# Kernel tuning notes

Hardware: AMD Instinct MI355X
Metric: run time of the kernel (lower is better)

Reference implementation:

```python
import jax, jax.numpy as jnp
import numpy as np


def euler2mat(angle):
    """angle: [..., 3] euler angles (x, y, z) -> [..., 3, 3] rotation matrix (xmat @ ymat @ zmat)."""
    x, y, z = angle[..., 0], angle[..., 1], angle[..., 2]
    zo = jnp.zeros_like(z)
    on = jnp.ones_like(z)
    cz, sz = jnp.cos(z), jnp.sin(z)
    cy, sy = jnp.cos(y), jnp.sin(y)
    cx, sx = jnp.cos(x), jnp.sin(x)
    zmat = jnp.stack([cz, -sz, zo, sz, cz, zo, zo, zo, on], axis=-1).reshape(*z.shape, 3, 3)
    ymat = jnp.stack([cy, zo, sy, zo, on, zo, -sy, zo, cy], axis=-1).reshape(*z.shape, 3, 3)
    xmat = jnp.stack([on, zo, zo, zo, cx, -sx, zo, sx, cx], axis=-1).reshape(*z.shape, 3, 3)
    return xmat @ ymat @ zmat


def pixel_grid(H, W, dtype=jnp.float32):
    """Matches torch affine_grid(identity, align_corners=False): normalized (x, y) in (-1, 1)."""
    xs = (2.0 * (jnp.arange(W, dtype=dtype) + 0.5) / W) - 1.0
    ys = (2.0 * (jnp.arange(H, dtype=dtype) + 0.5) / H) - 1.0
    X, Y = jnp.meshgrid(xs, ys, indexing='xy')  # [H, W] each
    return jnp.stack([X, Y], axis=-1)  # [H, W, 2], last dim = (x, y)


def setup_inputs() -> dict:
    key = jax.random.key(0)
    k1, k2, k3, k4, k5 = jax.random.split(key, 5)
    B, K, H, W = 8, 8, 384, 384
    im = jax.random.normal(k1, (B, H, W), dtype=jnp.float32)
    mask = jax.random.uniform(k2, (B, K, H, W), dtype=jnp.float32)
    depth = jax.random.uniform(k3, (B, H, W), dtype=jnp.float32, minval=0.5, maxval=1.5)
    T = jax.random.normal(k4, (B, K, 6), dtype=jnp.float32) * 0.1
    Tc = jax.random.normal(k5, (B, 9), dtype=jnp.float32) * 0.1
    return {"im": im, "mask": mask, "depth": depth, "T": T, "Tc": Tc}


def reference(im, mask, depth, T, Tc):
    B, K, H, W = mask.shape
    pixel = jnp.broadcast_to(pixel_grid(H, W, depth.dtype), (B, H, W, 2))  # [B,H,W,2]

    # object transforms
    t, a = T[..., 0:3], T[..., 3:6]            # [B,K,3] each
    R = euler2mat(a)                           # [B,K,3,3]
    # camera transform
    tc = Tc[..., 0:3]                          # [B,3]
    Rc = euler2mat(Tc[..., 3:6])               # [B,3,3]
    pc = Tc[..., 6:9]                          # [B,3]

    # pixel -> world (focal length = 1): [B,H,W,3]
    ones = jnp.ones((B, H, W, 1), dtype=depth.dtype)
    world = depth[..., None] * jnp.concatenate([pixel, ones], axis=-1)

    # centre of mass per mask: [B,K,3]
    total_mass = jnp.sum(mask, axis=(2, 3))[..., None] + 1e-6  # [B,K,1]
    p = jnp.einsum('bkhw,bhwc->bkc', mask, world) / total_mass

    # per-object rigid transform about centre of mass
    centered = world[:, None] - p[:, :, None, None]                       # [B,K,H,W,3]
    rotated = jnp.einsum('bkij,bkhwj->bkhwi', R, centered)                # [B,K,H,W,3]
    twc_k = rotated + (p + t)[:, :, None, None]                           # [B,K,H,W,3]

    # mask-weighted blend of per-object displacements
    twc = world + jnp.einsum('bkhw,bkhwc->bhwc', mask, twc_k - world[:, None])

    # camera transform about pivot pc
    twc = jnp.einsum('bij,bhwj->bhwi', Rc, twc - pc[:, None, None])
    twc = twc + (pc + tc)[:, None, None]

    # world -> pixel, flow
    new_pixel = twc[..., 0:2] / twc[..., 2:3]
    flow = new_pixel - pixel
    return flow
```

## Files before the change

### kernel.cpp

```cpp
#include <hip/hip_runtime.h>

#define B 8
#define K 8
#define H 384
#define W 384
#define HW (H*W)
#define NCPP 16
#define GROUPS_PER_B (HW/4)

#define WS_PK (B*K*NCPP*4)
#define WS_PB (WS_PK + B*K*12)

__device__ __forceinline__ void euler2mat(float ax, float ay, float az, float R[9]) {
    float cx = cosf(ax), sx = sinf(ax);
    float cy = cosf(ay), sy = sinf(ay);
    float cz = cosf(az), sz = sinf(az);
    R[0] = cy*cz;              R[1] = -cy*sz;             R[2] = sy;
    R[3] = cx*sz + sx*sy*cz;   R[4] = cx*cz - sx*sy*sz;   R[5] = -sx*cy;
    R[6] = sx*sz - cx*sy*cz;   R[7] = sx*cz + cx*sy*sz;   R[8] = cx*cy;
}

__global__ __launch_bounds__(256) void k_reduce(const float* __restrict__ mask,
                                                const float* __restrict__ depth,
                                                float* __restrict__ ws) {
    const int chunk = blockIdx.x, k = blockIdx.y, b = blockIdx.z;
    const int tid = threadIdx.x;

    const float4* m4 = (const float4*)(mask + ((size_t)(b*K + k)) * HW);
    const float4* d4 = (const float4*)(depth + (size_t)b * HW);

    float s0 = 0.f, s1 = 0.f, s2 = 0.f, s3 = 0.f;
    const float inv = 2.f / W;

#pragma unroll
    for (int r = 0; r < 9; ++r) {
        int g = (chunk * 9 + r) * 256 + tid;
        float4 mv = m4[g];
        float4 dv = d4[g];
        int i0 = g * 4;
        int h = i0 / W;
        int w0 = i0 - h * W;
        float py = 2.f * (h + 0.5f) * (1.f / H) - 1.f;
        float px0 = 2.f * (w0 + 0.5f) * (1.f / W) - 1.f;
        float mm[4] = {mv.x, mv.y, mv.z, mv.w};
        float dd[4] = {dv.x, dv.y, dv.z, dv.w};
#pragma unroll
        for (int j = 0; j < 4; ++j) {
            float m = mm[j];
            float t = m * dd[j];
            float px = px0 + j * inv;
            s0 += m; s1 += t * px; s2 += t * py; s3 += t;
        }
    }

    for (int off = 32; off > 0; off >>= 1) {
        s0 += __shfl_down(s0, off);
        s1 += __shfl_down(s1, off);
        s2 += __shfl_down(s2, off);
        s3 += __shfl_down(s3, off);
    }
    __shared__ float sd[16];
    int lane = tid & 63, wid = tid >> 6;
    if (lane == 0) { sd[wid*4+0]=s0; sd[wid*4+1]=s1; sd[wid*4+2]=s2; sd[wid*4+3]=s3; }
    __syncthreads();
    if (tid < 4) {
        float v = sd[tid] + sd[4 + tid] + sd[8 + tid] + sd[12 + tid];
        ws[(((b*K + k) * NCPP) + chunk) * 4 + tid] = v;
    }
}

__global__ void k_params(const float* __restrict__ T, const float* __restrict__ Tc,
                         float* __restrict__ ws) {
    int t = threadIdx.x;
    if (t < 64) {
        float s0 = 0.f, s1 = 0.f, s2 = 0.f, s3 = 0.f;
        for (int ch = 0; ch < NCPP; ++ch) {
            const float* src = ws + (t * NCPP + ch) * 4;
            s0 += src[0]; s1 += src[1]; s2 += src[2]; s3 += src[3];
        }
        float mass = s0 + 1e-6f;
        float p0 = s1 / mass, p1 = s2 / mass, p2 = s3 / mass;
        const float* Tk = T + t * 6;
        float R[9];
        euler2mat(Tk[3], Tk[4], Tk[5], R);
        float Rp0 = R[0]*p0 + R[1]*p1 + R[2]*p2;
        float Rp1 = R[3]*p0 + R[4]*p1 + R[5]*p2;
        float Rp2 = R[6]*p0 + R[7]*p1 + R[8]*p2;
        float* o = ws + WS_PK + t * 12;
        o[0] = R[0] - 1.f; o[1] = R[1];       o[2] = R[2];
        o[3] = R[3];       o[4] = R[4] - 1.f; o[5] = R[5];
        o[6] = R[6];       o[7] = R[7];       o[8] = R[8] - 1.f;
        o[9]  = p0 + Tk[0] - Rp0;
        o[10] = p1 + Tk[1] - Rp1;
        o[11] = p2 + Tk[2] - Rp2;
    }
    if (t < 8) {
        const float* Tb = Tc + t * 9;
        float R[9];
        euler2mat(Tb[3], Tb[4], Tb[5], R);
        float pc0 = Tb[6], pc1 = Tb[7], pc2 = Tb[8];
        float* o = ws + WS_PB + t * 12;
#pragma unroll
        for (int i = 0; i < 9; ++i) o[i] = R[i];
        o[9]  = pc0 + Tb[0] - (R[0]*pc0 + R[1]*pc1 + R[2]*pc2);
        o[10] = pc1 + Tb[1] - (R[3]*pc0 + R[4]*pc1 + R[5]*pc2);
        o[11] = pc2 + Tb[2] - (R[6]*pc0 + R[7]*pc1 + R[8]*pc2);
    }
}

__global__ __launch_bounds__(256) void k_flow(const float* __restrict__ mask,
                                              const float* __restrict__ depth,
                                              const float* __restrict__ ws,
                                              float* __restrict__ out) {
    const int b = blockIdx.y;
    const int tid = threadIdx.x;

    __shared__ float sp[108];
    if (tid < 96) sp[tid] = ws[WS_PK + b * 96 + tid];
    else if (tid < 108) sp[tid] = ws[WS_PB + b * 12 + (tid - 96)];
    __syncthreads();

    int g = blockIdx.x * 256 + tid;
    int i0 = g * 4;
    int h = i0 / W;
    int w0 = i0 - h * W;
    float py = 2.f * (h + 0.5f) * (1.f / H) - 1.f;
    const float inv = 2.f / W;
    float px0 = 2.f * (w0 + 0.5f) * (1.f / W) - 1.f;

    float4 dv = ((const float4*)(depth + (size_t)b * HW))[g];
    float4 mf[K];
#pragma unroll
    for (int k = 0; k < K; ++k)
        mf[k] = ((const float4*)(mask + ((size_t)(b*K + k)) * HW))[g];

    float dd[4] = {dv.x, dv.y, dv.z, dv.w};
    float res[8];
#pragma unroll
    for (int j = 0; j < 4; ++j) {
        float px = px0 + j * inv;
        float d = dd[j];
        float wx = d * px, wy = d * py, wz = d;
        float ax = wx, ay = wy, az = wz;
#pragma unroll
        for (int k = 0; k < K; ++k) {
            const float* P = sp + k * 12;
            float m = (j == 0) ? mf[k].x : (j == 1) ? mf[k].y : (j == 2) ? mf[k].z : mf[k].w;
            float rx = P[0]*wx + P[1]*wy + P[2]*wz + P[9];
            float ry = P[3]*wx + P[4]*wy + P[5]*wz + P[10];
            float rz = P[6]*wx + P[7]*wy + P[8]*wz + P[11];
            ax += m * rx; ay += m * ry; az += m * rz;
        }
        const float* C = sp + 96;
        float ox = C[0]*ax + C[1]*ay + C[2]*az + C[9];
        float oy = C[3]*ax + C[4]*ay + C[5]*az + C[10];
        float oz = C[6]*ax + C[7]*ay + C[8]*az + C[11];
        res[j*2 + 0] = ox / oz - px;
        res[j*2 + 1] = oy / oz - py;
    }

    float4* o4 = (float4*)(out + ((size_t)b * HW + i0) * 2);
    o4[0] = make_float4(res[0], res[1], res[2], res[3]);
    o4[1] = make_float4(res[4], res[5], res[6], res[7]);
}

extern "C" void kernel_launch(void* const* d_in, const int* in_sizes, int n_in,
                              void* d_out, int out_size, void* d_ws, size_t ws_size,
                              hipStream_t stream) {
    const float* mask  = (const float*)d_in[1];
    const float* depth = (const float*)d_in[2];
    const float* T     = (const float*)d_in[3];
    const float* Tc    = (const float*)d_in[4];
    float* ws  = (float*)d_ws;
    float* out = (float*)d_out;

    k_reduce<<<dim3(NCPP, K, B), 256, 0, stream>>>(mask, depth, ws);
    k_params<<<1, 64, 0, stream>>>(T, Tc, ws);
    k_flow<<<dim3(GROUPS_PER_B / 256, B), 256, 0, stream>>>(mask, depth, ws, out);
}
```

Measured before the change: 27.16 us.

## Restructure reduction to per-pixel-segment blocks loading all K masks at once

The reduction kernel now assigns each block one 256-float4 segment of one batch and loads all eight masks plus depth once per segment, reducing every mask's four moments in the same block. The old version used one block per (chunk, k, b) and reread depth for every mask. Partial sums are written per segment, 144 segments per batch, so the params kernel now serially sums 144 values per moment in a single block. The flow kernel uses a 1D grid matching the segment layout and writes its output with nontemporal stores. The extra serial summation in the one-block params kernel adds latency.

```diff
diff --git a/kernel.cpp b/kernel.cpp
--- a/kernel.cpp
+++ b/kernel.cpp
@@ -5,11 +5,13 @@
 #define H 384
 #define W 384
 #define HW (H*W)
-#define NCPP 16
-#define GROUPS_PER_B (HW/4)
+#define SEGS 144
+#define NBLK (B*SEGS)
+#define PBASE (B*32*SEGS)
+#define PB_CAM (PBASE + B*K*12)
 
-#define WS_PK (B*K*NCPP*4)
-#define WS_PB (WS_PK + B*K*12)
+typedef float f32x4 __attribute__((ext_vector_type(4)));
+
 
 __device__ __forceinline__ void euler2mat(float ax, float ay, float az, float R[9]) {
     float cx = cosf(ax), sx = sinf(ax);
@@ -20,52 +22,57 @@
     R[6] = sx*sz - cx*sy*cz;   R[7] = sx*cz + cx*sy*sz;   R[8] = cx*cy;
 }
 
-__global__ __launch_bounds__(256) void k_reduce(const float* __restrict__ mask,
-                                                const float* __restrict__ depth,
-                                                float* __restrict__ ws) {
-    const int chunk = blockIdx.x, k = blockIdx.y, b = blockIdx.z;
+__global__ __launch_bounds__(256) void k_pre(const float* __restrict__ mask,
+                                             const float* __restrict__ depth,
+                                             float* __restrict__ ws) {
     const int tid = threadIdx.x;
+    const int blk = blockIdx.x;
+    const int b = blk / SEGS;
+    const int seg = blk - b * SEGS;
+    const int g = seg * 256 + tid;
 
-    const float4* m4 = (const float4*)(mask + ((size_t)(b*K + k)) * HW);
-    const float4* d4 = (const float4*)(depth + (size_t)b * HW);
+    __shared__ float sred[128];
 
-    float s0 = 0.f, s1 = 0.f, s2 = 0.f, s3 = 0.f;
+    float4 mv[K];
+#pragma unroll
+    for (int k = 0; k < K; ++k)
+        mv[k] = ((const float4*)(mask + ((size_t)(b*K + k)) * HW))[g];
+    float4 dv = ((const float4*)(depth + (size_t)b * HW))[g];
+    float dd[4] = {dv.x, dv.y, dv.z, dv.w};
+
+    const int h = g / 96;
+    const int w0 = (g - h * 96) * 4;
+    const float py  = 2.f * (h + 0.5f) * (1.f / H) - 1.f;
+    const float px0 = 2.f * (w0 + 0.5f) * (1.f / W) - 1.f;
     const float inv = 2.f / W;
 
+    const int lane = tid & 63, wid = tid >> 6;
 #pragma unroll
-    for (int r = 0; r < 9; ++r) {
-        int g = (chunk * 9 + r) * 256 + tid;
-        float4 mv = m4[g];
-        float4 dv = d4[g];
-        int i0 = g * 4;
-        int h = i0 / W;
-        int w0 = i0 - h * W;
-        float py = 2.f * (h + 0.5f) * (1.f / H) - 1.f;
-        float px0 = 2.f * (w0 + 0.5f) * (1.f / W) - 1.f;
-        float mm[4] = {mv.x, mv.y, mv.z, mv.w};
-        float dd[4] = {dv.x, dv.y, dv.z, dv.w};
+    for (int k = 0; k < K; ++k) {
+        float mm[4] = {mv[k].x, mv[k].y, mv[k].z, mv[k].w};
+        float s0 = 0.f, s1 = 0.f, s2 = 0.f, s3 = 0.f;
 #pragma unroll
         for (int j = 0; j < 4; ++j) {
-            float m = mm[j];
-            float t = m * dd[j];
-            float px = px0 + j * inv;
+            float m = mm[j], t = m * dd[j], px = px0 + j * inv;
             s0 += m; s1 += t * px; s2 += t * py; s3 += t;
         }
+        for (int off = 32; off > 0; off >>= 1) {
+            s0 += __shfl_down(s0, off);
+            s1 += __shfl_down(s1, off);
+            s2 += __shfl_down(s2, off);
+            s3 += __shfl_down(s3, off);
+        }
+        if (lane == 0) {
+            sred[wid*32 + k*4 + 0] = s0;
+            sred[wid*32 + k*4 + 1] = s1;
+            sred[wid*32 + k*4 + 2] = s2;
+            sred[wid*32 + k*4 + 3] = s3;
+        }
     }
-
-    for (int off = 32; off > 0; off >>= 1) {
-        s0 += __shfl_down(s0, off);
-        s1 += __shfl_down(s1, off);
-        s2 += __shfl_down(s2, off);
-        s3 += __shfl_down(s3, off);
-    }
-    __shared__ float sd[16];
-    int lane = tid & 63, wid = tid >> 6;
-    if (lane == 0) { sd[wid*4+0]=s0; sd[wid*4+1]=s1; sd[wid*4+2]=s2; sd[wid*4+3]=s3; }
     __syncthreads();
-    if (tid < 4) {
-        float v = sd[tid] + sd[4 + tid] + sd[8 + tid] + sd[12 + tid];
-        ws[(((b*K + k) * NCPP) + chunk) * 4 + tid] = v;
+    if (tid < 32) {
+        float v = sred[tid] + sred[32 + tid] + sred[64 + tid] + sred[96 + tid];
+        ws[((size_t)(b*32 + tid)) * SEGS + seg] = v;
     }
 }
 
@@ -73,20 +80,24 @@
                          float* __restrict__ ws) {
     int t = threadIdx.x;
     if (t < 64) {
-        float s0 = 0.f, s1 = 0.f, s2 = 0.f, s3 = 0.f;
-        for (int ch = 0; ch < NCPP; ++ch) {
-            const float* src = ws + (t * NCPP + ch) * 4;
-            s0 += src[0]; s1 += src[1]; s2 += src[2]; s3 += src[3];
+        int b = t >> 3, k = t & 7;
+        float s[4];
+#pragma unroll
+        for (int c = 0; c < 4; ++c) {
+            const float* src = ws + ((size_t)(b*32 + k*4 + c)) * SEGS;
+            float acc = 0.f;
+            for (int sg = 0; sg < SEGS; ++sg) acc += src[sg];
+            s[c] = acc;
         }
-        float mass = s0 + 1e-6f;
-        float p0 = s1 / mass, p1 = s2 / mass, p2 = s3 / mass;
+        float mass = s[0] + 1e-6f;
+        float p0 = s[1] / mass, p1 = s[2] / mass, p2 = s[3] / mass;
         const float* Tk = T + t * 6;
         float R[9];
         euler2mat(Tk[3], Tk[4], Tk[5], R);
         float Rp0 = R[0]*p0 + R[1]*p1 + R[2]*p2;
         float Rp1 = R[3]*p0 + R[4]*p1 + R[5]*p2;
         float Rp2 = R[6]*p0 + R[7]*p1 + R[8]*p2;
-        float* o = ws + WS_PK + t * 12;
+        float* o = ws + PBASE + t * 12;
         o[0] = R[0] - 1.f; o[1] = R[1];       o[2] = R[2];
         o[3] = R[3];       o[4] = R[4] - 1.f; o[5] = R[5];
         o[6] = R[6];       o[7] = R[7];       o[8] = R[8] - 1.f;
@@ -99,7 +110,7 @@
         float R[9];
         euler2mat(Tb[3], Tb[4], Tb[5], R);
         float pc0 = Tb[6], pc1 = Tb[7], pc2 = Tb[8];
-        float* o = ws + WS_PB + t * 12;
+        float* o = ws + PB_CAM + t * 12;
 #pragma unroll
         for (int i = 0; i < 9; ++i) o[i] = R[i];
         o[9]  = pc0 + Tb[0] - (R[0]*pc0 + R[1]*pc1 + R[2]*pc2);
@@ -112,27 +123,29 @@
                                               const float* __restrict__ depth,
                                               const float* __restrict__ ws,
                                               float* __restrict__ out) {
-    const int b = blockIdx.y;
     const int tid = threadIdx.x;
+    const int blk = blockIdx.x;
+    const int b = blk / SEGS;
+    const int seg = blk - b * SEGS;
+    const int g = seg * 256 + tid;
 
     __shared__ float sp[108];
-    if (tid < 96) sp[tid] = ws[WS_PK + b * 96 + tid];
-    else if (tid < 108) sp[tid] = ws[WS_PB + b * 12 + (tid - 96)];
+    if (tid < 96) sp[tid] = ws[PBASE + b * 96 + tid];
+    else if (tid < 108) sp[tid] = ws[PB_CAM + b * 12 + (tid - 96)];
     __syncthreads();
-
-    int g = blockIdx.x * 256 + tid;
-    int i0 = g * 4;
-    int h = i0 / W;
-    int w0 = i0 - h * W;
-    float py = 2.f * (h + 0.5f) * (1.f / H) - 1.f;
-    const float inv = 2.f / W;
-    float px0 = 2.f * (w0 + 0.5f) * (1.f / W) - 1.f;
 
     float4 dv = ((const float4*)(depth + (size_t)b * HW))[g];
     float4 mf[K];
 #pragma unroll
     for (int k = 0; k < K; ++k)
         mf[k] = ((const float4*)(mask + ((size_t)(b*K + k)) * HW))[g];
+
+    const int i0 = g * 4;
+    const int h = i0 / W;
+    const int w0 = i0 - h * W;
+    const float py = 2.f * (h + 0.5f) * (1.f / H) - 1.f;
+    const float inv = 2.f / W;
+    const float px0 = 2.f * (w0 + 0.5f) * (1.f / W) - 1.f;
 
     float dd[4] = {dv.x, dv.y, dv.z, dv.w};
     float res[8];
@@ -159,9 +172,11 @@
         res[j*2 + 1] = oy / oz - py;
     }
 
-    float4* o4 = (float4*)(out + ((size_t)b * HW + i0) * 2);
-    o4[0] = make_float4(res[0], res[1], res[2], res[3]);
-    o4[1] = make_float4(res[4], res[5], res[6], res[7]);
+    f32x4* o4 = (f32x4*)(out + ((size_t)b * HW + i0) * 2);
+    f32x4 v0 = {res[0], res[1], res[2], res[3]};
+    f32x4 v1 = {res[4], res[5], res[6], res[7]};
+    __builtin_nontemporal_store(v0, o4);
+    __builtin_nontemporal_store(v1, o4 + 1);
 }
 
 extern "C" void kernel_launch(void* const* d_in, const int* in_sizes, int n_in,
@@ -174,7 +189,7 @@
     float* ws  = (float*)d_ws;
     float* out = (float*)d_out;
 
-    k_reduce<<<dim3(NCPP, K, B), 256, 0, stream>>>(mask, depth, ws);
+    k_pre<<<NBLK, 256, 0, stream>>>(mask, depth, ws);
     k_params<<<1, 64, 0, stream>>>(T, Tc, ws);
-    k_flow<<<dim3(GROUPS_PER_B / 256, B), 256, 0, stream>>>(mask, depth, ws, out);
+    k_flow<<<NBLK, 256, 0, stream>>>(mask, depth, ws, out);
 }
```

Measured after the change: 40.08 us. 1.48x slower.

## Add nontemporal mask loads/stores and process three pixel groups per flow thread

Applied to the files above, without the earlier changes.

Mask reads in the reduction and flow kernels now use nontemporal loads, and flow outputs use nontemporal stores, to reduce cache pollution from streaming data. The flow kernel is restructured to 384-thread blocks where each thread handles three float4 groups. The mask loop is interchanged so that one mask plane is loaded for all three groups at a time. Depth loads are issued before the barrier to overlap with the parameter copy. The grid shrinks to 32 blocks per batch, which may lower occupancy and add register pressure.

```diff
diff --git a/kernel.cpp b/kernel.cpp
--- a/kernel.cpp
+++ b/kernel.cpp
@@ -7,9 +7,15 @@
 #define HW (H*W)
 #define NCPP 16
 #define GROUPS_PER_B (HW/4)
-
 #define WS_PK (B*K*NCPP*4)
 #define WS_PB (WS_PK + B*K*12)
+
+typedef float f32x4 __attribute__((ext_vector_type(4)));
+
+__device__ __forceinline__ float4 ntload4(const float* p) {
+    f32x4 v = __builtin_nontemporal_load((const f32x4*)p);
+    return make_float4(v.x, v.y, v.z, v.w);
+}
 
 __device__ __forceinline__ void euler2mat(float ax, float ay, float az, float R[9]) {
     float cx = cosf(ax), sx = sinf(ax);
@@ -26,7 +32,7 @@
     const int chunk = blockIdx.x, k = blockIdx.y, b = blockIdx.z;
     const int tid = threadIdx.x;
 
-    const float4* m4 = (const float4*)(mask + ((size_t)(b*K + k)) * HW);
+    const float* mbase = mask + ((size_t)(b*K + k)) * HW;
     const float4* d4 = (const float4*)(depth + (size_t)b * HW);
 
     float s0 = 0.f, s1 = 0.f, s2 = 0.f, s3 = 0.f;
@@ -35,7 +41,7 @@
 #pragma unroll
     for (int r = 0; r < 9; ++r) {
         int g = (chunk * 9 + r) * 256 + tid;
-        float4 mv = m4[g];
+        float4 mv = ntload4(mbase + (size_t)g * 4);
         float4 dv = d4[g];
         int i0 = g * 4;
         int h = i0 / W;
@@ -83,16 +89,13 @@
         const float* Tk = T + t * 6;
         float R[9];
         euler2mat(Tk[3], Tk[4], Tk[5], R);
-        float Rp0 = R[0]*p0 + R[1]*p1 + R[2]*p2;
-        float Rp1 = R[3]*p0 + R[4]*p1 + R[5]*p2;
-        float Rp2 = R[6]*p0 + R[7]*p1 + R[8]*p2;
         float* o = ws + WS_PK + t * 12;
         o[0] = R[0] - 1.f; o[1] = R[1];       o[2] = R[2];
         o[3] = R[3];       o[4] = R[4] - 1.f; o[5] = R[5];
         o[6] = R[6];       o[7] = R[7];       o[8] = R[8] - 1.f;
-        o[9]  = p0 + Tk[0] - Rp0;
-        o[10] = p1 + Tk[1] - Rp1;
-        o[11] = p2 + Tk[2] - Rp2;
+        o[9]  = p0 + Tk[0] - (R[0]*p0 + R[1]*p1 + R[2]*p2);
+        o[10] = p1 + Tk[1] - (R[3]*p0 + R[4]*p1 + R[5]*p2);
+        o[11] = p2 + Tk[2] - (R[6]*p0 + R[7]*p1 + R[8]*p2);
     }
     if (t < 8) {
         const float* Tb = Tc + t * 9;
@@ -108,60 +111,89 @@
     }
 }
 
-__global__ __launch_bounds__(256) void k_flow(const float* __restrict__ mask,
-                                              const float* __restrict__ depth,
-                                              const float* __restrict__ ws,
-                                              float* __restrict__ out) {
+__global__ __launch_bounds__(384) void k_flow3(const float* __restrict__ mask,
+                                               const float* __restrict__ depth,
+                                               const float* __restrict__ ws,
+                                               float* __restrict__ out) {
     const int b = blockIdx.y;
+    const int wdw = blockIdx.x;
     const int tid = threadIdx.x;
 
     __shared__ float sp[108];
     if (tid < 96) sp[tid] = ws[WS_PK + b * 96 + tid];
     else if (tid < 108) sp[tid] = ws[WS_PB + b * 12 + (tid - 96)];
+
+    int g[3];
+    float4 dvv[3];
+#pragma unroll
+    for (int i = 0; i < 3; ++i) {
+        g[i] = wdw * 1152 + i * 384 + tid;
+        dvv[i] = ((const float4*)(depth + (size_t)b * HW))[g[i]];
+    }
     __syncthreads();
 
-    int g = blockIdx.x * 256 + tid;
-    int i0 = g * 4;
-    int h = i0 / W;
-    int w0 = i0 - h * W;
-    float py = 2.f * (h + 0.5f) * (1.f / H) - 1.f;
     const float inv = 2.f / W;
-    float px0 = 2.f * (w0 + 0.5f) * (1.f / W) - 1.f;
-
-    float4 dv = ((const float4*)(depth + (size_t)b * HW))[g];
-    float4 mf[K];
-#pragma unroll
-    for (int k = 0; k < K; ++k)
-        mf[k] = ((const float4*)(mask + ((size_t)(b*K + k)) * HW))[g];
-
-    float dd[4] = {dv.x, dv.y, dv.z, dv.w};
-    float res[8];
-#pragma unroll
-    for (int j = 0; j < 4; ++j) {
-        float px = px0 + j * inv;
-        float d = dd[j];
-        float wx = d * px, wy = d * py, wz = d;
-        float ax = wx, ay = wy, az = wz;
-#pragma unroll
-        for (int k = 0; k < K; ++k) {
-            const float* P = sp + k * 12;
-            float m = (j == 0) ? mf[k].x : (j == 1) ? mf[k].y : (j == 2) ? mf[k].z : mf[k].w;
-            float rx = P[0]*wx + P[1]*wy + P[2]*wz + P[9];
-            float ry = P[3]*wx + P[4]*wy + P[5]*wz + P[10];
-            float rz = P[6]*wx + P[7]*wy + P[8]*wz + P[11];
-            ax += m * rx; ay += m * ry; az += m * rz;
-        }
-        const float* C = sp + 96;
-        float ox = C[0]*ax + C[1]*ay + C[2]*az + C[9];
-        float oy = C[3]*ax + C[4]*ay + C[5]*az + C[10];
-        float oz = C[6]*ax + C[7]*ay + C[8]*az + C[11];
-        res[j*2 + 0] = ox / oz - px;
-        res[j*2 + 1] = oy / oz - py;
-    }
-
-    float4* o4 = (float4*)(out + ((size_t)b * HW + i0) * 2);
-    o4[0] = make_float4(res[0], res[1], res[2], res[3]);
-    o4[1] = make_float4(res[4], res[5], res[6], res[7]);
+    float pyv[3], pxj[3][4], dd[3][4];
+    float wx[3][4], wy[3][4], wz[3][4], ax[3][4], ay[3][4], az[3][4];
+#pragma unroll
+    for (int i = 0; i < 3; ++i) {
+        int h = g[i] / 96;
+        int w0 = (g[i] - h * 96) * 4;
+        pyv[i] = 2.f * (h + 0.5f) * (1.f / H) - 1.f;
+        float px0 = 2.f * (w0 + 0.5f) * (1.f / W) - 1.f;
+        float d4a[4] = {dvv[i].x, dvv[i].y, dvv[i].z, dvv[i].w};
+#pragma unroll
+        for (int j = 0; j < 4; ++j) {
+            pxj[i][j] = px0 + j * inv;
+            dd[i][j] = d4a[j];
+            wx[i][j] = d4a[j] * pxj[i][j];
+            wy[i][j] = d4a[j] * pyv[i];
+            wz[i][j] = d4a[j];
+            ax[i][j] = wx[i][j]; ay[i][j] = wy[i][j]; az[i][j] = wz[i][j];
+        }
+    }
+
+    const float* mb = mask + ((size_t)b * K) * HW;
+#pragma unroll
+    for (int k = 0; k < K; ++k) {
+        const float* P = sp + k * 12;
+        float4 mv[3];
+#pragma unroll
+        for (int i = 0; i < 3; ++i)
+            mv[i] = ntload4(mb + (size_t)k * HW + (size_t)g[i] * 4);
+#pragma unroll
+        for (int i = 0; i < 3; ++i) {
+            float mm[4] = {mv[i].x, mv[i].y, mv[i].z, mv[i].w};
+#pragma unroll
+            for (int j = 0; j < 4; ++j) {
+                float rx = P[0]*wx[i][j] + P[1]*wy[i][j] + P[2]*wz[i][j] + P[9];
+                float ry = P[3]*wx[i][j] + P[4]*wy[i][j] + P[5]*wz[i][j] + P[10];
+                float rz = P[6]*wx[i][j] + P[7]*wy[i][j] + P[8]*wz[i][j] + P[11];
+                ax[i][j] += mm[j] * rx;
+                ay[i][j] += mm[j] * ry;
+                az[i][j] += mm[j] * rz;
+            }
+        }
+    }
+
+    const float* C = sp + 96;
+#pragma unroll
+    for (int i = 0; i < 3; ++i) {
+        float res[8];
+#pragma unroll
+        for (int j = 0; j < 4; ++j) {
+            float ox = C[0]*ax[i][j] + C[1]*ay[i][j] + C[2]*az[i][j] + C[9];
+            float oy = C[3]*ax[i][j] + C[4]*ay[i][j] + C[5]*az[i][j] + C[10];
+            float oz = C[6]*ax[i][j] + C[7]*ay[i][j] + C[8]*az[i][j] + C[11];
+            res[j*2 + 0] = ox / oz - pxj[i][j];
+            res[j*2 + 1] = oy / oz - pyv[i];
+        }
+        f32x4* o4 = (f32x4*)(out + ((size_t)b * HW + (size_t)g[i] * 4) * 2);
+        f32x4 v0 = {res[0], res[1], res[2], res[3]};
+        f32x4 v1 = {res[4], res[5], res[6], res[7]};
+        __builtin_nontemporal_store(v0, o4);
+        __builtin_nontemporal_store(v1, o4 + 1);
+    }
 }
 
 extern "C" void kernel_launch(void* const* d_in, const int* in_sizes, int n_in,
@@ -176,5 +208,5 @@
 
     k_reduce<<<dim3(NCPP, K, B), 256, 0, stream>>>(mask, depth, ws);
     k_params<<<1, 64, 0, stream>>>(T, Tc, ws);
-    k_flow<<<dim3(GROUPS_PER_B / 256, B), 256, 0, stream>>>(mask, depth, ws, out);
-}
+    k_flow3<<<dim3(32, B), 384, 0, stream>>>(mask, depth, ws, out);
+}
```

Result: no change. 27.13 us (-0.1%).
